# Kernel tuning notes

Measured on AMD Instinct MI355X. Metric: run time of the kernel, lower is better.

Reference implementation:

```python
import jax, jax.numpy as jnp
import numpy as np

KSIZE = 3
COUT = 128
GC = 4

def _unfold(x, k):
    # x: [B,C,H,W] -> [B,C,k*k,H,W]; zero pad (k-1)//2, stride 1 (matches nn.Unfold ordering)
    B, C, H, W = x.shape
    p = (k - 1) // 2
    xp = jnp.pad(x, ((0, 0), (0, 0), (p, p), (p, p)))
    return jnp.stack([xp[:, :, i:i + H, j:j + W] for i in range(k) for j in range(k)], axis=2)

def _bn(x, g, b, m, v, eps=1e-5):
    # inference-mode BatchNorm along channel axis 1, any rank
    sh = (1, -1) + (1,) * (x.ndim - 2)
    return (x - m.reshape(sh)) * (g / jnp.sqrt(v + eps)).reshape(sh) + b.reshape(sh)

def setup_inputs():
    key = jax.random.key(0)
    ks = jax.random.split(key, 15)
    B, C, H, W = 4, 128, 56, 56
    mid = C // 4
    OG = COUT * GC
    s = 0.05
    return {
        'x': jax.random.normal(ks[0], (B, C, H, W), jnp.float32),
        'Wk': jax.random.normal(ks[1], (C, C), jnp.float32) * s,
        'bn1_g': jax.random.uniform(ks[2], (C,), jnp.float32, 0.5, 1.5),
        'bn1_b': jax.random.normal(ks[3], (C,), jnp.float32) * s,
        'bn1_m': jnp.zeros((C,), jnp.float32),
        'bn1_v': jnp.ones((C,), jnp.float32),
        'W1': jax.random.normal(ks[4], (mid, 2 * C), jnp.float32) * s,
        'b1': jax.random.normal(ks[5], (mid,), jnp.float32) * s,
        'bn2_g': jax.random.uniform(ks[6], (mid,), jnp.float32, 0.5, 1.5),
        'bn2_b': jax.random.normal(ks[7], (mid,), jnp.float32) * s,
        'bn2_m': jnp.zeros((mid,), jnp.float32),
        'bn2_v': jnp.ones((mid,), jnp.float32),
        'W2': jax.random.normal(ks[8], (OG, mid), jnp.float32) * s,
        'b2': jax.random.normal(ks[9], (OG,), jnp.float32) * s,
        'gn_g': jax.random.uniform(ks[10], (OG,), jnp.float32, 0.5, 1.5),
        'gn_b': jax.random.normal(ks[11], (OG,), jnp.float32) * s,
        'Wv': jax.random.normal(ks[12], (OG, C), jnp.float32) * s,
        'bnv_g': jax.random.uniform(ks[13], (OG,), jnp.float32, 0.5, 1.5),
        'bnv_b': jax.random.normal(ks[14], (OG,), jnp.float32) * s,
        'bnv_m': jnp.zeros((OG,), jnp.float32),
        'bnv_v': jnp.ones((OG,), jnp.float32),
    }

def reference(x, Wk, bn1_g, bn1_b, bn1_m, bn1_v, W1, b1, bn2_g, bn2_b, bn2_m, bn2_v,
              W2, b2, gn_g, gn_b, Wv, bnv_g, bnv_b, bnv_m, bnv_v):
    B, C, H, W = x.shape
    k2 = KSIZE * KSIZE
    # emb_K: 1x1 conv (no bias) + BN + ReLU, then local unfold
    ke = jax.nn.relu(_bn(jnp.einsum('bchw,dc->bdhw', x, Wk), bn1_g, bn1_b, bn1_m, bn1_v))
    Kp = _unfold(ke, KSIZE)                        # [B,C,k2,H,W]
    Q = jnp.broadcast_to(x[:, :, None], Kp.shape)  # repeat x over k2 (einops '(c k)')
    QK = jnp.concatenate([Q, Kp], axis=1)          # [B,2C,k2,H,W]
    # MLP: 1x1 convs act pointwise over (k2,H,W)
    h = jax.nn.relu(_bn(jnp.einsum('bcphw,mc->bmphw', QK, W1) + b1.reshape(1, -1, 1, 1, 1),
                        bn2_g, bn2_b, bn2_m, bn2_v))
    a = jnp.einsum('bmphw,om->bophw', h, W2) + b2.reshape(1, -1, 1, 1, 1)  # [B,COUT*GC,k2,H,W]
    a = a.reshape(B, COUT, GC, k2, H, W)
    # GroupNorm: num_groups=COUT -> normalize over (GC, k2, H, W) per (b, out)
    mu = a.mean(axis=(2, 3, 4, 5), keepdims=True)
    var = jnp.mean(jnp.square(a - mu), axis=(2, 3, 4, 5), keepdims=True)
    a = (a - mu) / jnp.sqrt(var + 1e-5)
    a = a * gn_g.reshape(1, COUT, GC, 1, 1, 1) + gn_b.reshape(1, COUT, GC, 1, 1, 1)
    # emb_V: 1x1 conv (no bias) + BN, then local unfold
    v = _bn(jnp.einsum('bchw,oc->bohw', x, Wv), bnv_g, bnv_b, bnv_m, bnv_v)
    V = _unfold(v, KSIZE).reshape(B, COUT, GC, k2, H, W)
    return jnp.sum(a * V, axis=(2, 3))             # [B,COUT,H,W]
```

## Files before the change

### kernel.cpp

```cpp
#include <hip/hip_runtime.h>
#include <hip/hip_bf16.h>

typedef __hip_bfloat16 bf16;
typedef __attribute__((ext_vector_type(8))) short short8;
typedef __attribute__((ext_vector_type(4))) float f32x4;

#define HWP 3136
#define WD 56
#define PW 58
#define PADP 3364
#define CC 128
#define MIDM 32
#define OGN 512
#define NB 4

enum : int {
  OFF_FLAG = 0,
  OFF_W2F  = 4,
  OFF_SC2  = OFF_W2F + OGN*MIDM,
  OFF_SH2  = OFF_SC2 + MIDM,
  OFF_B1F  = OFF_SH2 + MIDM,
  OFF_B2F  = OFF_B1F + MIDM,
  OFF_GNG  = OFF_B2F + OGN,
  OFF_GNB  = OFF_GNG + OGN,
  OFF_GPART= OFF_GNB + OGN,
  OFF_PQ   = OFF_GPART + NB*128*1056,
  OFF_SS1  = OFF_PQ + NB*OGN*2,
  OFF_SSV  = OFF_SS1 + CC*2,
  OFF_WKB  = OFF_SSV + OGN*2,
  OFF_WVB  = OFF_WKB + CC*CC/2,
  OFF_W1AB = OFF_WVB + OGN*CC/2,
  OFF_W1BB = OFF_W1AB + MIDM*CC/2,
  OFF_HQT  = OFF_W1BB + MIDM*CC/2,
  OFF_GKT  = OFF_HQT + NB*HWP*MIDM/2,
  OFF_VT   = OFF_GKT + NB*PADP*MIDM/2,
  OFF_R1   = OFF_VT + NB*PADP*OGN/2,
  OFF_XT   = OFF_R1,
  WS_TOTAL = OFF_R1 + NB*9*HWP*MIDM/2
};

__device__ __forceinline__ float b2f(unsigned short u) {
  bf16 h; *(unsigned short*)&h = u; return __bfloat162float(h);
}
__device__ __forceinline__ unsigned short f2b(float f) {
  bf16 h = __float2bfloat16(f); return *(unsigned short*)&h;
}
__device__ __forceinline__ float ldmix(const void* p, size_t i, bool isbf) {
  return isbf ? __bfloat162float(((const bf16*)p)[i]) : ((const float*)p)[i];
}
__device__ __forceinline__ f32x4 mfma16(short8 a, short8 b, f32x4 c) {
  return __builtin_amdgcn_mfma_f32_16x16x32_bf16(a, b, c, 0, 0, 0);
}
__device__ __forceinline__ bool detect_bf(const unsigned short* xr) {
  int cnt = 0;
#pragma unroll
  for (int i = 0; i < 32; i++) {
    short8 v = *(const short8*)(xr + i*8);
#pragma unroll
    for (int j = 0; j < 8; j++) {
      int e = (((unsigned short)v[j]) >> 7) & 0xFF;
      cnt += (e >= 141) ? 1 : 0;
    }
  }
  return cnt < 8;
}

__global__ __launch_bounds__(256) void k_prep(
    const void* __restrict__ x,  const void* __restrict__ Wk,
    const void* __restrict__ bn1_g, const void* __restrict__ bn1_b,
    const void* __restrict__ bn1_m, const void* __restrict__ bn1_v,
    const void* __restrict__ W1, const void* __restrict__ b1,
    const void* __restrict__ bn2_g, const void* __restrict__ bn2_b,
    const void* __restrict__ bn2_m, const void* __restrict__ bn2_v,
    const void* __restrict__ W2, const void* __restrict__ b2,
    const void* __restrict__ gn_g, const void* __restrict__ gn_b,
    const void* __restrict__ Wv,
    const void* __restrict__ bnv_g, const void* __restrict__ bnv_b,
    const void* __restrict__ bnv_m, const void* __restrict__ bnv_v,
    float* __restrict__ ws) {
  __shared__ unsigned short tile[32*130];
  const bool isbf = detect_bf((const unsigned short*)x);
  int blk = blockIdx.x, tid = threadIdx.x;
  if (blk == 0 && tid == 0) ws[OFF_FLAG] = isbf ? 1.f : 0.f;
  int gid = blk*256 + tid, gstride = gridDim.x*256;
  unsigned short* wkb = (unsigned short*)(ws + OFF_WKB);
  unsigned short* wvb = (unsigned short*)(ws + OFF_WVB);
  unsigned short* w1ab = (unsigned short*)(ws + OFF_W1AB);
  unsigned short* w1bb = (unsigned short*)(ws + OFF_W1BB);
  float2* ss1 = (float2*)(ws + OFF_SS1);
  float2* ssv = (float2*)(ws + OFF_SSV);
  for (int i = gid; i < CC*CC; i += gstride) wkb[i] = f2b(ldmix(Wk, i, isbf));
  for (int i = gid; i < OGN*CC; i += gstride) wvb[i] = f2b(ldmix(Wv, i, isbf));
  for (int i = gid; i < MIDM*CC; i += gstride) {
    int m = i / CC, c = i % CC;
    w1ab[i] = f2b(ldmix(W1, (size_t)m*(2*CC) + c, isbf));
    w1bb[i] = f2b(ldmix(W1, (size_t)m*(2*CC) + CC + c, isbf));
  }
  for (int i = gid; i < OGN*MIDM; i += gstride) ws[OFF_W2F + i] = ldmix(W2, i, isbf);
  for (int i = gid; i < CC; i += gstride) {
    float s = ldmix(bn1_g, i, isbf) / sqrtf(ldmix(bn1_v, i, isbf) + 1e-5f);
    ss1[i] = make_float2(s, ldmix(bn1_b, i, isbf) - ldmix(bn1_m, i, isbf) * s);
  }
  for (int i = gid; i < MIDM; i += gstride) {
    float s = ldmix(bn2_g, i, isbf) / sqrtf(ldmix(bn2_v, i, isbf) + 1e-5f);
    ws[OFF_SC2 + i] = s;
    ws[OFF_SH2 + i] = ldmix(bn2_b, i, isbf) - ldmix(bn2_m, i, isbf)*s;
    ws[OFF_B1F + i] = ldmix(b1, i, isbf);
  }
  for (int i = gid; i < OGN; i += gstride) {
    float s = ldmix(bnv_g, i, isbf) / sqrtf(ldmix(bnv_v, i, isbf) + 1e-5f);
    ssv[i] = make_float2(s, ldmix(bnv_b, i, isbf) - ldmix(bnv_m, i, isbf) * s);
    ws[OFF_B2F + i] = ldmix(b2, i, isbf);
    ws[OFF_GNG + i] = ldmix(gn_g, i, isbf);
    ws[OFF_GNB + i] = ldmix(gn_b, i, isbf);
  }
  if (blk < 392) {
    int b = blk / 98, pix0 = (blk % 98)*32;
#pragma unroll
    for (int k = 0; k < 16; k++) {
      int idx = tid + k*256;
      int c = idx >> 5, pl = idx & 31;
      tile[pl*130 + c] = f2b(ldmix(x, ((size_t)b*CC + c)*HWP + pix0 + pl, isbf));
    }
    __syncthreads();
    unsigned short* xt = (unsigned short*)(ws + OFF_XT);
#pragma unroll
    for (int k = 0; k < 16; k++) {
      int idx = tid + k*256;
      int c = idx & 127, pl = idx >> 7;
      xt[((size_t)b*HWP + pix0 + pl)*CC + c] = tile[pl*130 + c];
    }
  } else {
    const int NV = 912*64, NG = NB*PADP*4;
    const short8 z = {0,0,0,0,0,0,0,0};
    unsigned short* vt = (unsigned short*)(ws + OFF_VT);
    unsigned short* gk = (unsigned short*)(ws + OFF_GKT);
    for (int u = (blk-392)*256 + tid; u < NV + NG; u += 28*256) {
      if (u < NV) {
        int bpp = u >> 6, och = u & 63;
        int b = bpp / 228, j = bpp - b*228;
        int pp;
        if (j < 58)       pp = j;
        else if (j < 116) pp = 57*PW + (j - 58);
        else if (j < 172) pp = (j - 116 + 1)*PW;
        else              pp = (j - 172 + 1)*PW + 57;
        *(short8*)(vt + ((size_t)b*PADP + pp)*OGN + och*8) = z;
      } else {
        int u2 = u - NV;
        int b = u2 / (PADP*4), rem = u2 - b*(PADP*4);
        int pp = rem >> 2, mch = rem & 3;
        *(short8*)(gk + ((size_t)b*PADP + pp)*MIDM + mch*8) = z;
      }
    }
  }
}

__global__ __launch_bounds__(256, 4) void k_mid(float* __restrict__ ws) {
  __shared__ unsigned short keL[4][16][136];
  int bid = blockIdx.x, tid = threadIdx.x;
  int w = tid >> 6, lane = tid & 63, q = lane >> 4, l16 = lane & 15;
  if (bid < 196) {
    int b = bid / 49, bx = bid - (bid/49)*49;
    int pix = bx*64 + w*16 + l16;
    const unsigned short* xt = (const unsigned short*)(ws + OFF_XT) + ((size_t)b*HWP + pix)*CC;
    short8 Bx[4];
#pragma unroll
    for (int kk = 0; kk < 4; kk++) Bx[kk] = *(const short8*)(xt + kk*32 + q*8);
    const unsigned short* wkb = (const unsigned short*)(ws + OFF_WKB);
    const float2* ss = (const float2*)(ws + OFF_SS1);
#pragma unroll
    for (int ot = 0; ot < 8; ot++) {
      int drow = ot*16 + l16;
      f32x4 c = {0.f, 0.f, 0.f, 0.f};
#pragma unroll
      for (int kk = 0; kk < 4; kk++)
        c = mfma16(*(const short8*)(wkb + (size_t)drow*CC + kk*32 + q*8), Bx[kk], c);
      int d0 = ot*16 + q*4;
      ushort4 st;
      { float2 s = ss[d0+0]; st.x = f2b(fmaxf(s.x*c[0] + s.y, 0.f)); }
      { float2 s = ss[d0+1]; st.y = f2b(fmaxf(s.x*c[1] + s.y, 0.f)); }
      { float2 s = ss[d0+2]; st.z = f2b(fmaxf(s.x*c[2] + s.y, 0.f)); }
      { float2 s = ss[d0+3]; st.w = f2b(fmaxf(s.x*c[3] + s.y, 0.f)); }
      *(ushort4*)&keL[w][l16][d0] = st;
    }
    __syncthreads();
    short8 Bk[4];
#pragma unroll
    for (int kk = 0; kk < 4; kk++) Bk[kk] = *(const short8*)&keL[w][l16][kk*32 + q*8];
    const unsigned short* w1a = (const unsigned short*)(ws + OFF_W1AB);
    const unsigned short* w1b = (const unsigned short*)(ws + OFF_W1BB);
    int h0 = pix / WD, w0 = pix - h0*WD;
    int pp = (h0+1)*PW + (w0+1);
    unsigned short* hqt = (unsigned short*)(ws + OFF_HQT) + ((size_t)b*HWP + pix)*MIDM;
    unsigned short* gkt = (unsigned short*)(ws + OFF_GKT) + ((size_t)b*PADP + pp)*MIDM;
#pragma unroll
    for (int mt = 0; mt < 2; mt++) {
      int mrow = mt*16 + l16;
      f32x4 ch = {0.f,0.f,0.f,0.f}, cg = {0.f,0.f,0.f,0.f};
#pragma unroll
      for (int kk = 0; kk < 4; kk++) {
        ch = mfma16(*(const short8*)(w1a + (size_t)mrow*CC + kk*32 + q*8), Bx[kk], ch);
        cg = mfma16(*(const short8*)(w1b + (size_t)mrow*CC + kk*32 + q*8), Bk[kk], cg);
      }
      int m0 = mt*16 + q*4;
      ushort4 sh, sg;
      sh.x = f2b(ch[0]); sh.y = f2b(ch[1]); sh.z = f2b(ch[2]); sh.w = f2b(ch[3]);
      sg.x = f2b(cg[0]); sg.y = f2b(cg[1]); sg.z = f2b(cg[2]); sg.w = f2b(cg[3]);
      *(ushort4*)(hqt + m0) = sh;
      *(ushort4*)(gkt + m0) = sg;
    }
  } else {
    int vid = bid - 196;
    int bx = vid % 49, rest = vid / 49;
    int by = rest & 3, b = rest >> 2;
    int pix = bx*64 + w*16 + l16;
    int h0 = pix / WD, w0 = pix - h0*WD;
    int pp = (h0+1)*PW + (w0+1);
    const unsigned short* xt = (const unsigned short*)(ws + OFF_XT) + ((size_t)b*HWP + pix)*CC;
    short8 B[4];
#pragma unroll
    for (int kk = 0; kk < 4; kk++) B[kk] = *(const short8*)(xt + kk*32 + q*8);
    const unsigned short* wvb = (const unsigned short*)(ws + OFF_WVB);
    const float2* ss = (const float2*)(ws + OFF_SSV);
    unsigned short* vt = (unsigned short*)(ws + OFF_VT) + ((size_t)b*PADP + pp)*OGN;
#pragma unroll
    for (int ot = 0; ot < 8; ot++) {
      int orow = by*128 + ot*16 + l16;
      f32x4 c = {0.f, 0.f, 0.f, 0.f};
#pragma unroll
      for (int kk = 0; kk < 4; kk++)
        c = mfma16(*(const short8*)(wvb + (size_t)orow*CC + kk*32 + q*8), B[kk], c);
      int o0 = by*128 + ot*16 + q*4;
      ushort4 st;
      { float2 s = ss[o0+0]; st.x = f2b(s.x*c[0] + s.y); }
      { float2 s = ss[o0+1]; st.y = f2b(s.x*c[1] + s.y); }
      { float2 s = ss[o0+2]; st.z = f2b(s.x*c[2] + s.y); }
      { float2 s = ss[o0+3]; st.w = f2b(s.x*c[3] + s.y); }
      *(ushort4*)(vt + o0) = st;
    }
  }
}

__global__ __launch_bounds__(256) void k_gramh(float* __restrict__ ws) {
  __shared__ unsigned short tileT[32][264];
  int b = blockIdx.y, bk = blockIdx.x;
  int tid = threadIdx.x;
  int w = tid >> 6, lane = tid & 63, q = lane >> 4, l16 = lane & 15;
  const int base = bk * 882;
  const unsigned short* hqt = (const unsigned short*)(ws + OFF_HQT) + (size_t)b*HWP*MIDM;
  const unsigned short* gkp = (const unsigned short*)(ws + OFF_GKT) + (size_t)b*PADP*MIDM;
  float sc2[MIDM], bas0[MIDM];
#pragma unroll
  for (int m = 0; m < MIDM; m++) {
    sc2[m] = ws[OFF_SC2 + m];
    bas0[m] = sc2[m]*ws[OFF_B1F + m] + ws[OFF_SH2 + m];
  }
  f32x4 gLL={0,0,0,0}, gLH={0,0,0,0}, gHH={0,0,0,0}, sL={0,0,0,0}, sH={0,0,0,0};
  short8 ones;
#pragma unroll
  for (int j = 0; j < 8; j++) ones[j] = (short)0x3F80;
  for (int t = 0; t < 4; t++) {
    int r = t*256 + tid;
    bool valid = r < 882;
    int R = valid ? (base + r) : 0;
    int p = R / HWP, pix = R - p*HWP;
    int h0 = pix / WD, w0 = pix - h0*WD;
    int npp = (h0 + p/3)*PW + (w0 + p - (p/3)*3);
    const unsigned short* hq = hqt + (size_t)pix*MIDM;
    const unsigned short* gk = gkp + (size_t)npp*MIDM;
#pragma unroll
    for (int ch = 0; ch < 4; ch++) {
      short8 th = *(const short8*)(hq + ch*8);
      short8 tg = *(const short8*)(gk + ch*8);
      short8 o;
#pragma unroll
      for (int j = 0; j < 8; j++) {
        int m = ch*8 + j;
        float hv = b2f((unsigned short)th[j]) + b2f((unsigned short)tg[j]);
        float v = fmaxf(sc2[m]*hv + bas0[m], 0.f);
        o[j] = valid ? (short)f2b(v) : (short)0;
      }
#pragma unroll
      for (int j = 0; j < 8; j++) tileT[ch*8 + j][tid] = (unsigned short)o[j];
    }
    __syncthreads();
#pragma unroll
    for (int cc = 0; cc < 2; cc++) {
      int c = w*2 + cc;
      short8 alo = *(const short8*)&tileT[l16][c*32 + q*8];
      short8 ahi = *(const short8*)&tileT[l16+16][c*32 + q*8];
      gLL = mfma16(alo, alo, gLL);
      gLH = mfma16(alo, ahi, gLH);
      gHH = mfma16(ahi, ahi, gHH);
      sL = mfma16(alo, ones, sL);
      sH = mfma16(ahi, ones, sH);
    }
    __syncthreads();
  }
  float* blob = ws + OFF_GPART + ((size_t)((b*32 + bk)*4 + w))*1056;
#pragma unroll
  for (int r = 0; r < 4; r++) {
    int row = q*4 + r;
    blob[row*32 + l16]             = gLL[r];
    blob[row*32 + 16 + l16]        = gLH[r];
    blob[(16 + l16)*32 + row]      = gLH[r];
    blob[(16 + row)*32 + 16 + l16] = gHH[r];
  }
  if (l16 == 0) {
#pragma unroll
    for (int r = 0; r < 4; r++) {
      blob[1024 + q*4 + r]      = sL[r];
      blob[1024 + 16 + q*4 + r] = sH[r];
    }
  }
}

__global__ __launch_bounds__(512) void k_stats(float* __restrict__ ws) {
  __shared__ float Gs[MIDM*MIDM], S1s[MIDM], saS[OGN], sqS[OGN], muS[128], invS[128];
  int b = blockIdx.x, o = threadIdx.x;
  for (int e = o; e < 1056; e += 512) {
    float s = 0.f;
    const float* pb = ws + OFF_GPART + (size_t)b*128*1056 + e;
    for (int p = 0; p < 128; p++) s += pb[(size_t)p*1056];
    if (e < 1024) Gs[e] = s; else S1s[e - 1024] = s;
  }
  __syncthreads();
  float w2[MIDM];
#pragma unroll
  for (int m = 0; m < MIDM; m++) w2[m] = ws[OFF_W2F + o*MIDM + m];
  float dotS = 0.f;
#pragma unroll
  for (int m = 0; m < MIDM; m++) dotS += w2[m] * S1s[m];
  float quad = 0.f;
  for (int a = 0; a < MIDM; a++) {
    float t = 0.f;
#pragma unroll
    for (int c = 0; c < MIDM; c++) t += Gs[a*MIDM + c] * w2[c];
    quad += w2[a] * t;
  }
  float b2o = ws[OFF_B2F + o];
  const float M = 9.f * HWP;
  saS[o] = dotS + b2o * M;
  sqS[o] = quad + 2.f*b2o*dotS + b2o*b2o*M;
  __syncthreads();
  if (o < 128) {
    float sa = saS[4*o] + saS[4*o+1] + saS[4*o+2] + saS[4*o+3];
    float sq = sqS[4*o] + sqS[4*o+1] + sqS[4*o+2] + sqS[4*o+3];
    const float invN = 1.f / (4.f * M);
    float mu = sa * invN;
    float var = sq * invN - mu*mu;
    muS[o] = mu;
    invS[o] = 1.f / sqrtf(var + 1e-5f);
  }
  __syncthreads();
  int co = o >> 2;
  float alpha = ws[OFF_GNG + o] * invS[co];
  ((float2*)(ws + OFF_PQ))[b*OGN + o] =
      make_float2(alpha, alpha*b2o + ws[OFF_GNB + o] - muS[co]*alpha);
}

#define VST2 68
__global__ __launch_bounds__(256, 5) void k_out(const float* __restrict__ ws,
                                                void* __restrict__ outp) {
  __shared__ unsigned short tileV[192*VST2];
  int b = blockIdx.z, by = blockIdx.y;
  int tid = threadIdx.x;
  int w = tid >> 6, lane = tid & 63, q = lane >> 4, l16 = lane & 15;
  int pix0 = blockIdx.x*64;
  int h00 = pix0 / WD, w00 = pix0 - h00*WD;
  int wstart = (h00+1)*PW + (w00+1) - (PW+1);
  int pix = pix0 + w*16 + l16;
  int h0 = pix / WD, w0 = pix - h0*WD;
  const unsigned short* hq = (const unsigned short*)(ws + OFF_HQT)
      + ((size_t)b*HWP + pix)*MIDM + q*8;
  const unsigned short* gkb = (const unsigned short*)(ws + OFF_GKT)
      + ((size_t)b*PADP + h0*PW + w0)*MIDM + q*8;
  float sc[8], ba[8], hvq[8];
  {
    short8 th = *(const short8*)hq;
#pragma unroll
    for (int j = 0; j < 8; j++) {
      int m = q*8 + j;
      sc[j] = ws[OFF_SC2 + m];
      ba[j] = sc[j]*ws[OFF_B1F + m] + ws[OFF_SH2 + m];
      hvq[j] = b2f((unsigned short)th[j]);
    }
  }
  short8 Bf[9];
#pragma unroll
  for (int p = 0; p < 9; p++) {
    short8 tg = *(const short8*)(gkb + (size_t)((p/3)*PW + (p - (p/3)*3))*MIDM);
#pragma unroll
    for (int j = 0; j < 8; j++)
      Bf[p][j] = (short)f2b(fmaxf(sc[j]*(hvq[j] + b2f((unsigned short)tg[j])) + ba[j], 0.f));
  }
  const unsigned short* vsrc = (const unsigned short*)(ws + OFF_VT)
      + (size_t)b*PADP*OGN + (size_t)by*64;
#pragma unroll
  for (int i = 0; i < 12; i++) {
    int u = i*256 + tid;
    int wp = u >> 4, col = (u & 15)*4;
    *(ushort4*)&tileV[wp*VST2 + col] =
        *(const ushort4*)(vsrc + (size_t)(wstart + wp)*OGN + col);
  }
  const bool isbf = ws[OFF_FLAG] > 0.5f;
  const float2* pq = (const float2*)(ws + OFF_PQ) + b*OGN;
  short8 A[4];
  f32x4 Qv[4];
#pragma unroll
  for (int ot = 0; ot < 4; ot++) {
    int orow = by*64 + ot*16 + l16;
    float P = pq[orow].x;
    const float* wrow = ws + OFF_W2F + (size_t)orow*MIDM + q*8;
    short8 a;
#pragma unroll
    for (int j = 0; j < 8; j++) a[j] = (short)f2b(P * wrow[j]);
    A[ot] = a;
    int o0 = by*64 + ot*16 + q*4;
    f32x4 qv = { pq[o0+0].y, pq[o0+1].y, pq[o0+2].y, pq[o0+3].y };
    Qv[ot] = qv;
  }
  int ppl = (h0+1)*PW + (w0+1) - wstart;
  float acc[4];
#pragma unroll
  for (int ot = 0; ot < 4; ot++) acc[ot] = 0.f;
  __syncthreads();
  const int doff[9] = {-PW-1, -PW, -PW+1, -1, 0, 1, PW-1, PW, PW+1};
#pragma unroll
  for (int p = 0; p < 9; p++) {
    int lp = ppl + doff[p];
    const unsigned short* vrow = &tileV[lp*VST2];
#pragma unroll
    for (int ot = 0; ot < 4; ot++) {
      f32x4 c = {0.f, 0.f, 0.f, 0.f};
      c = mfma16(A[ot], Bf[p], c);
      ushort4 vv = *(const ushort4*)(vrow + ot*16 + q*4);
      acc[ot] += (c[0] + Qv[ot][0])*b2f(vv.x) + (c[1] + Qv[ot][1])*b2f(vv.y)
               + (c[2] + Qv[ot][2])*b2f(vv.z) + (c[3] + Qv[ot][3])*b2f(vv.w);
    }
  }
#pragma unroll
  for (int ot = 0; ot < 4; ot++) {
    int co = by*16 + ot*4 + q;
    size_t oidx = ((size_t)b*128 + co)*HWP + pix;
    if (isbf) __builtin_nontemporal_store(f2b(acc[ot]), (unsigned short*)outp + oidx);
    else      __builtin_nontemporal_store(acc[ot], (float*)outp + oidx);
  }
}

extern "C" void kernel_launch(void* const* d_in, const int* in_sizes, int n_in,
                              void* d_out, int out_size, void* d_ws, size_t ws_size,
                              hipStream_t stream) {
  float* ws = (float*)d_ws;
  hipLaunchKernelGGL(k_prep, dim3(420), dim3(256), 0, stream,
                     d_in[0], d_in[1], d_in[2], d_in[3], d_in[4], d_in[5],
                     d_in[6], d_in[7], d_in[8], d_in[9], d_in[10], d_in[11],
                     d_in[12], d_in[13], d_in[14], d_in[15], d_in[16],
                     d_in[17], d_in[18], d_in[19], d_in[20], ws);
  hipLaunchKernelGGL(k_mid,  dim3(980),      dim3(256), 0, stream, ws);
  hipLaunchKernelGGL(k_gramh,dim3(32, 4),    dim3(256), 0, stream, ws);
  hipLaunchKernelGGL(k_stats,dim3(4),        dim3(512), 0, stream, ws);
  hipLaunchKernelGGL(k_out,  dim3(49, 8, 4), dim3(256), 0, stream, ws, d_out);
}
```

Baseline: 225.3 us.

## Process two pixel tiles per k_out block and precompute scaled W2 in k_stats

Each k_out block now covers 128 pixels instead of 64, staging a larger V tile in shared memory so the A fragments, Q values and scale constants are loaded once and reused for both halves. The GroupNorm-scaled W2 matrix (alpha*W2) is now converted to bf16 once in k_stats and stored in the workspace, replacing per-block float loads and conversions. This trades more shared memory and lower occupancy (launch bounds drop from 5 to 4) and a serial second half for less redundant setup work and halo reloading.

```diff
diff --git a/kernel.cpp b/kernel.cpp
--- a/kernel.cpp
+++ b/kernel.cpp
@@ -36,6 +36,7 @@
   OFF_VT   = OFF_GKT + NB*PADP*MIDM/2,
   OFF_R1   = OFF_VT + NB*PADP*OGN/2,
   OFF_XT   = OFF_R1,
+  OFF_AB   = OFF_R1,
   WS_TOTAL = OFF_R1 + NB*9*HWP*MIDM/2
 };
 
@@ -357,47 +358,58 @@
   float alpha = ws[OFF_GNG + o] * invS[co];
   ((float2*)(ws + OFF_PQ))[b*OGN + o] =
       make_float2(alpha, alpha*b2o + ws[OFF_GNB + o] - muS[co]*alpha);
+  unsigned short* dst = (unsigned short*)(ws + OFF_AB) + ((size_t)b*OGN + o)*MIDM;
+#pragma unroll
+  for (int m = 0; m < MIDM; m += 4) {
+    ushort4 t;
+    t.x = f2b(alpha*w2[m+0]); t.y = f2b(alpha*w2[m+1]);
+    t.z = f2b(alpha*w2[m+2]); t.w = f2b(alpha*w2[m+3]);
+    *(ushort4*)(dst + m) = t;
+  }
 }
 
 #define VST2 68
-__global__ __launch_bounds__(256, 5) void k_out(const float* __restrict__ ws,
+__global__ __launch_bounds__(256, 4) void k_out(const float* __restrict__ ws,
                                                 void* __restrict__ outp) {
-  __shared__ unsigned short tileV[192*VST2];
+  __shared__ unsigned short tileV[256*VST2];
   int b = blockIdx.z, by = blockIdx.y;
+  int bx = blockIdx.x;
   int tid = threadIdx.x;
   int w = tid >> 6, lane = tid & 63, q = lane >> 4, l16 = lane & 15;
-  int pix0 = blockIdx.x*64;
+  int pix0 = bx*128;
   int h00 = pix0 / WD, w00 = pix0 - h00*WD;
   int wstart = (h00+1)*PW + (w00+1) - (PW+1);
-  int pix = pix0 + w*16 + l16;
-  int h0 = pix / WD, w0 = pix - h0*WD;
-  const unsigned short* hq = (const unsigned short*)(ws + OFF_HQT)
-      + ((size_t)b*HWP + pix)*MIDM + q*8;
-  const unsigned short* gkb = (const unsigned short*)(ws + OFF_GKT)
-      + ((size_t)b*PADP + h0*PW + w0)*MIDM + q*8;
-  float sc[8], ba[8], hvq[8];
+  const bool hasB = (bx < 24);
+  int pixA = pix0 + w*16 + l16;
+  float sc[8], ba[8];
+#pragma unroll
+  for (int j = 0; j < 8; j++) {
+    int m = q*8 + j;
+    sc[j] = ws[OFF_SC2 + m];
+    ba[j] = sc[j]*ws[OFF_B1F + m] + ws[OFF_SH2 + m];
+  }
+  const unsigned short* hqt = (const unsigned short*)(ws + OFF_HQT) + (size_t)b*HWP*MIDM;
+  const unsigned short* gkt = (const unsigned short*)(ws + OFF_GKT) + (size_t)b*PADP*MIDM;
+  int hA = pixA / WD, wA = pixA - hA*WD;
+  short8 BfA[9];
   {
-    short8 th = *(const short8*)hq;
-#pragma unroll
-    for (int j = 0; j < 8; j++) {
-      int m = q*8 + j;
-      sc[j] = ws[OFF_SC2 + m];
-      ba[j] = sc[j]*ws[OFF_B1F + m] + ws[OFF_SH2 + m];
-      hvq[j] = b2f((unsigned short)th[j]);
-    }
-  }
-  short8 Bf[9];
-#pragma unroll
-  for (int p = 0; p < 9; p++) {
-    short8 tg = *(const short8*)(gkb + (size_t)((p/3)*PW + (p - (p/3)*3))*MIDM);
-#pragma unroll
-    for (int j = 0; j < 8; j++)
-      Bf[p][j] = (short)f2b(fmaxf(sc[j]*(hvq[j] + b2f((unsigned short)tg[j])) + ba[j], 0.f));
+    short8 th = *(const short8*)(hqt + (size_t)pixA*MIDM + q*8);
+    float hv[8];
+#pragma unroll
+    for (int j = 0; j < 8; j++) hv[j] = b2f((unsigned short)th[j]);
+    const unsigned short* gkb = gkt + ((size_t)hA*PW + wA)*MIDM + q*8;
+#pragma unroll
+    for (int p = 0; p < 9; p++) {
+      short8 tg = *(const short8*)(gkb + (size_t)((p/3)*PW + (p - (p/3)*3))*MIDM);
+#pragma unroll
+      for (int j = 0; j < 8; j++)
+        BfA[p][j] = (short)f2b(fmaxf(sc[j]*(hv[j] + b2f((unsigned short)tg[j])) + ba[j], 0.f));
+    }
   }
   const unsigned short* vsrc = (const unsigned short*)(ws + OFF_VT)
       + (size_t)b*PADP*OGN + (size_t)by*64;
 #pragma unroll
-  for (int i = 0; i < 12; i++) {
+  for (int i = 0; i < 16; i++) {
     int u = i*256 + tid;
     int wp = u >> 4, col = (u & 15)*4;
     *(ushort4*)&tileV[wp*VST2 + col] =
@@ -405,46 +417,83 @@
   }
   const bool isbf = ws[OFF_FLAG] > 0.5f;
   const float2* pq = (const float2*)(ws + OFF_PQ) + b*OGN;
+  const unsigned short* ABp = (const unsigned short*)(ws + OFF_AB)
+      + ((size_t)b*OGN + by*64)*MIDM;
   short8 A[4];
   f32x4 Qv[4];
 #pragma unroll
   for (int ot = 0; ot < 4; ot++) {
-    int orow = by*64 + ot*16 + l16;
-    float P = pq[orow].x;
-    const float* wrow = ws + OFF_W2F + (size_t)orow*MIDM + q*8;
-    short8 a;
-#pragma unroll
-    for (int j = 0; j < 8; j++) a[j] = (short)f2b(P * wrow[j]);
-    A[ot] = a;
+    A[ot] = *(const short8*)(ABp + (size_t)(ot*16 + l16)*MIDM + q*8);
     int o0 = by*64 + ot*16 + q*4;
     f32x4 qv = { pq[o0+0].y, pq[o0+1].y, pq[o0+2].y, pq[o0+3].y };
     Qv[ot] = qv;
   }
-  int ppl = (h0+1)*PW + (w0+1) - wstart;
-  float acc[4];
-#pragma unroll
-  for (int ot = 0; ot < 4; ot++) acc[ot] = 0.f;
+  const int doff[9] = {-PW-1, -PW, -PW+1, -1, 0, 1, PW-1, PW, PW+1};
   __syncthreads();
-  const int doff[9] = {-PW-1, -PW, -PW+1, -1, 0, 1, PW-1, PW, PW+1};
-#pragma unroll
-  for (int p = 0; p < 9; p++) {
-    int lp = ppl + doff[p];
-    const unsigned short* vrow = &tileV[lp*VST2];
+  {
+    int ppl = (hA+1)*PW + (wA+1) - wstart;
+    float acc[4] = {0.f, 0.f, 0.f, 0.f};
+#pragma unroll
+    for (int p = 0; p < 9; p++) {
+      int lp = ppl + doff[p];
+      const unsigned short* vrow = &tileV[lp*VST2];
+#pragma unroll
+      for (int ot = 0; ot < 4; ot++) {
+        f32x4 c = {0.f, 0.f, 0.f, 0.f};
+        c = mfma16(A[ot], BfA[p], c);
+        ushort4 vv = *(const ushort4*)(vrow + ot*16 + q*4);
+        acc[ot] += (c[0] + Qv[ot][0])*b2f(vv.x) + (c[1] + Qv[ot][1])*b2f(vv.y)
+                 + (c[2] + Qv[ot][2])*b2f(vv.z) + (c[3] + Qv[ot][3])*b2f(vv.w);
+      }
+    }
 #pragma unroll
     for (int ot = 0; ot < 4; ot++) {
-      f32x4 c = {0.f, 0.f, 0.f, 0.f};
-      c = mfma16(A[ot], Bf[p], c);
-      ushort4 vv = *(const ushort4*)(vrow + ot*16 + q*4);
-      acc[ot] += (c[0] + Qv[ot][0])*b2f(vv.x) + (c[1] + Qv[ot][1])*b2f(vv.y)
-               + (c[2] + Qv[ot][2])*b2f(vv.z) + (c[3] + Qv[ot][3])*b2f(vv.w);
-    }
-  }
-#pragma unroll
-  for (int ot = 0; ot < 4; ot++) {
-    int co = by*16 + ot*4 + q;
-    size_t oidx = ((size_t)b*128 + co)*HWP + pix;
-    if (isbf) __builtin_nontemporal_store(f2b(acc[ot]), (unsigned short*)outp + oidx);
-    else      __builtin_nontemporal_store(acc[ot], (float*)outp + oidx);
+      int co = by*16 + ot*4 + q;
+      size_t oidx = ((size_t)b*128 + co)*HWP + pixA;
+      if (isbf) __builtin_nontemporal_store(f2b(acc[ot]), (unsigned short*)outp + oidx);
+      else      __builtin_nontemporal_store(acc[ot], (float*)outp + oidx);
+    }
+  }
+  if (hasB) {
+    int pixB = pixA + 64;
+    int hB = pixB / WD, wB = pixB - hB*WD;
+    short8 BfB[9];
+    {
+      short8 th = *(const short8*)(hqt + (size_t)pixB*MIDM + q*8);
+      float hv[8];
+#pragma unroll
+      for (int j = 0; j < 8; j++) hv[j] = b2f((unsigned short)th[j]);
+      const unsigned short* gkb = gkt + ((size_t)hB*PW + wB)*MIDM + q*8;
+#pragma unroll
+      for (int p = 0; p < 9; p++) {
+        short8 tg = *(const short8*)(gkb + (size_t)((p/3)*PW + (p - (p/3)*3))*MIDM);
+#pragma unroll
+        for (int j = 0; j < 8; j++)
+          BfB[p][j] = (short)f2b(fmaxf(sc[j]*(hv[j] + b2f((unsigned short)tg[j])) + ba[j], 0.f));
+      }
+    }
+    int ppl = (hB+1)*PW + (wB+1) - wstart;
+    float acc[4] = {0.f, 0.f, 0.f, 0.f};
+#pragma unroll
+    for (int p = 0; p < 9; p++) {
+      int lp = ppl + doff[p];
+      const unsigned short* vrow = &tileV[lp*VST2];
+#pragma unroll
+      for (int ot = 0; ot < 4; ot++) {
+        f32x4 c = {0.f, 0.f, 0.f, 0.f};
+        c = mfma16(A[ot], BfB[p], c);
+        ushort4 vv = *(const ushort4*)(vrow + ot*16 + q*4);
+        acc[ot] += (c[0] + Qv[ot][0])*b2f(vv.x) + (c[1] + Qv[ot][1])*b2f(vv.y)
+                 + (c[2] + Qv[ot][2])*b2f(vv.z) + (c[3] + Qv[ot][3])*b2f(vv.w);
+      }
+    }
+#pragma unroll
+    for (int ot = 0; ot < 4; ot++) {
+      int co = by*16 + ot*4 + q;
+      size_t oidx = ((size_t)b*128 + co)*HWP + pixB;
+      if (isbf) __builtin_nontemporal_store(f2b(acc[ot]), (unsigned short*)outp + oidx);
+      else      __builtin_nontemporal_store(acc[ot], (float*)outp + oidx);
+    }
   }
 }
 
@@ -460,5 +509,5 @@
   hipLaunchKernelGGL(k_mid,  dim3(980),      dim3(256), 0, stream, ws);
   hipLaunchKernelGGL(k_gramh,dim3(32, 4),    dim3(256), 0, stream, ws);
   hipLaunchKernelGGL(k_stats,dim3(4),        dim3(512), 0, stream, ws);
-  hipLaunchKernelGGL(k_out,  dim3(49, 8, 4), dim3(256), 0, stream, ws, d_out);
-}
+  hipLaunchKernelGGL(k_out,  dim3(25, 8, 4), dim3(256), 0, stream, ws, d_out);
+}
```

Result: faster. 213.7 us (-5.1%).

## Process two output-channel tiles per k_out block and precompute scaled bf16 W2

Applied to the files above, without the earlier changes.

Each k_out block now covers 128 output groups (two passes of 64) rather than 64, so the per-pixel ReLU'd B fragments built from the HQ/GK buffers are computed once and reused across twice as many channels, and the grid's y dimension halves. The GroupNorm-scaled W2 matrix is now converted to bf16 once in k_stats and stored in the reused R1 workspace region, replacing the per-block scale-and-convert work. The V tile in shared memory doubles in width and the launch-bounds occupancy hint drops from 5 to 3, trading occupancy and parallelism for less redundant work.

```diff
diff --git a/kernel.cpp b/kernel.cpp
--- a/kernel.cpp
+++ b/kernel.cpp
@@ -36,6 +36,7 @@
   OFF_VT   = OFF_GKT + NB*PADP*MIDM/2,
   OFF_R1   = OFF_VT + NB*PADP*OGN/2,
   OFF_XT   = OFF_R1,
+  OFF_AB   = OFF_R1,
   WS_TOTAL = OFF_R1 + NB*9*HWP*MIDM/2
 };
 
@@ -357,94 +358,100 @@
   float alpha = ws[OFF_GNG + o] * invS[co];
   ((float2*)(ws + OFF_PQ))[b*OGN + o] =
       make_float2(alpha, alpha*b2o + ws[OFF_GNB + o] - muS[co]*alpha);
-}
-
-#define VST2 68
-__global__ __launch_bounds__(256, 5) void k_out(const float* __restrict__ ws,
+  unsigned short* dst = (unsigned short*)(ws + OFF_AB) + ((size_t)b*OGN + o)*MIDM;
+#pragma unroll
+  for (int m = 0; m < MIDM; m += 4) {
+    ushort4 t;
+    t.x = f2b(alpha*w2[m+0]); t.y = f2b(alpha*w2[m+1]);
+    t.z = f2b(alpha*w2[m+2]); t.w = f2b(alpha*w2[m+3]);
+    *(ushort4*)(dst + m) = t;
+  }
+}
+
+#define VST 136
+__global__ __launch_bounds__(256, 3) void k_out(const float* __restrict__ ws,
                                                 void* __restrict__ outp) {
-  __shared__ unsigned short tileV[192*VST2];
-  int b = blockIdx.z, by = blockIdx.y;
+  __shared__ unsigned short tileV[192*VST];
+  int b = blockIdx.z, bp = blockIdx.y;
+  int bx = blockIdx.x;
   int tid = threadIdx.x;
   int w = tid >> 6, lane = tid & 63, q = lane >> 4, l16 = lane & 15;
-  int pix0 = blockIdx.x*64;
+  int pix0 = bx*64;
   int h00 = pix0 / WD, w00 = pix0 - h00*WD;
   int wstart = (h00+1)*PW + (w00+1) - (PW+1);
   int pix = pix0 + w*16 + l16;
+  float sc[8], ba[8];
+#pragma unroll
+  for (int j = 0; j < 8; j++) {
+    int m = q*8 + j;
+    sc[j] = ws[OFF_SC2 + m];
+    ba[j] = sc[j]*ws[OFF_B1F + m] + ws[OFF_SH2 + m];
+  }
+  const unsigned short* hqt = (const unsigned short*)(ws + OFF_HQT) + (size_t)b*HWP*MIDM;
+  const unsigned short* gkt = (const unsigned short*)(ws + OFF_GKT) + (size_t)b*PADP*MIDM;
   int h0 = pix / WD, w0 = pix - h0*WD;
-  const unsigned short* hq = (const unsigned short*)(ws + OFF_HQT)
-      + ((size_t)b*HWP + pix)*MIDM + q*8;
-  const unsigned short* gkb = (const unsigned short*)(ws + OFF_GKT)
-      + ((size_t)b*PADP + h0*PW + w0)*MIDM + q*8;
-  float sc[8], ba[8], hvq[8];
+  short8 Bf[9];
   {
-    short8 th = *(const short8*)hq;
-#pragma unroll
-    for (int j = 0; j < 8; j++) {
-      int m = q*8 + j;
-      sc[j] = ws[OFF_SC2 + m];
-      ba[j] = sc[j]*ws[OFF_B1F + m] + ws[OFF_SH2 + m];
-      hvq[j] = b2f((unsigned short)th[j]);
-    }
-  }
-  short8 Bf[9];
-#pragma unroll
-  for (int p = 0; p < 9; p++) {
-    short8 tg = *(const short8*)(gkb + (size_t)((p/3)*PW + (p - (p/3)*3))*MIDM);
-#pragma unroll
-    for (int j = 0; j < 8; j++)
-      Bf[p][j] = (short)f2b(fmaxf(sc[j]*(hvq[j] + b2f((unsigned short)tg[j])) + ba[j], 0.f));
+    short8 th = *(const short8*)(hqt + (size_t)pix*MIDM + q*8);
+    float hv[8];
+#pragma unroll
+    for (int j = 0; j < 8; j++) hv[j] = b2f((unsigned short)th[j]);
+    const unsigned short* gkb = gkt + ((size_t)h0*PW + w0)*MIDM + q*8;
+#pragma unroll
+    for (int p = 0; p < 9; p++) {
+      short8 tg = *(const short8*)(gkb + (size_t)((p/3)*PW + (p - (p/3)*3))*MIDM);
+#pragma unroll
+      for (int j = 0; j < 8; j++)
+        Bf[p][j] = (short)f2b(fmaxf(sc[j]*(hv[j] + b2f((unsigned short)tg[j])) + ba[j], 0.f));
+    }
   }
   const unsigned short* vsrc = (const unsigned short*)(ws + OFF_VT)
-      + (size_t)b*PADP*OGN + (size_t)by*64;
+      + (size_t)b*PADP*OGN + (size_t)bp*128;
 #pragma unroll
   for (int i = 0; i < 12; i++) {
     int u = i*256 + tid;
-    int wp = u >> 4, col = (u & 15)*4;
-    *(ushort4*)&tileV[wp*VST2 + col] =
-        *(const ushort4*)(vsrc + (size_t)(wstart + wp)*OGN + col);
+    int wp = u >> 4, col = (u & 15)*8;
+    *(short8*)&tileV[wp*VST + col] =
+        *(const short8*)(vsrc + (size_t)(wstart + wp)*OGN + col);
   }
   const bool isbf = ws[OFF_FLAG] > 0.5f;
   const float2* pq = (const float2*)(ws + OFF_PQ) + b*OGN;
-  short8 A[4];
-  f32x4 Qv[4];
-#pragma unroll
-  for (int ot = 0; ot < 4; ot++) {
-    int orow = by*64 + ot*16 + l16;
-    float P = pq[orow].x;
-    const float* wrow = ws + OFF_W2F + (size_t)orow*MIDM + q*8;
-    short8 a;
-#pragma unroll
-    for (int j = 0; j < 8; j++) a[j] = (short)f2b(P * wrow[j]);
-    A[ot] = a;
-    int o0 = by*64 + ot*16 + q*4;
-    f32x4 qv = { pq[o0+0].y, pq[o0+1].y, pq[o0+2].y, pq[o0+3].y };
-    Qv[ot] = qv;
-  }
+  const unsigned short* ABb = (const unsigned short*)(ws + OFF_AB)
+      + ((size_t)b*OGN + bp*128)*MIDM;
+  const int doff[9] = {-PW-1, -PW, -PW+1, -1, 0, 1, PW-1, PW, PW+1};
   int ppl = (h0+1)*PW + (w0+1) - wstart;
-  float acc[4];
-#pragma unroll
-  for (int ot = 0; ot < 4; ot++) acc[ot] = 0.f;
   __syncthreads();
-  const int doff[9] = {-PW-1, -PW, -PW+1, -1, 0, 1, PW-1, PW, PW+1};
-#pragma unroll
-  for (int p = 0; p < 9; p++) {
-    int lp = ppl + doff[p];
-    const unsigned short* vrow = &tileV[lp*VST2];
+  for (int byv = 0; byv < 2; ++byv) {
+    short8 A[4];
+    f32x4 Qv[4];
 #pragma unroll
     for (int ot = 0; ot < 4; ot++) {
-      f32x4 c = {0.f, 0.f, 0.f, 0.f};
-      c = mfma16(A[ot], Bf[p], c);
-      ushort4 vv = *(const ushort4*)(vrow + ot*16 + q*4);
-      acc[ot] += (c[0] + Qv[ot][0])*b2f(vv.x) + (c[1] + Qv[ot][1])*b2f(vv.y)
-               + (c[2] + Qv[ot][2])*b2f(vv.z) + (c[3] + Qv[ot][3])*b2f(vv.w);
-    }
-  }
-#pragma unroll
-  for (int ot = 0; ot < 4; ot++) {
-    int co = by*16 + ot*4 + q;
-    size_t oidx = ((size_t)b*128 + co)*HWP + pix;
-    if (isbf) __builtin_nontemporal_store(f2b(acc[ot]), (unsigned short*)outp + oidx);
-    else      __builtin_nontemporal_store(acc[ot], (float*)outp + oidx);
+      A[ot] = *(const short8*)(ABb + (size_t)(byv*64 + ot*16 + l16)*MIDM + q*8);
+      int o0 = bp*128 + byv*64 + ot*16 + q*4;
+      f32x4 qv = { pq[o0+0].y, pq[o0+1].y, pq[o0+2].y, pq[o0+3].y };
+      Qv[ot] = qv;
+    }
+    float acc[4] = {0.f, 0.f, 0.f, 0.f};
+#pragma unroll
+    for (int p = 0; p < 9; p++) {
+      int lp = ppl + doff[p];
+      const unsigned short* vrow = &tileV[lp*VST + byv*64];
+#pragma unroll
+      for (int ot = 0; ot < 4; ot++) {
+        f32x4 c = {0.f, 0.f, 0.f, 0.f};
+        c = mfma16(A[ot], Bf[p], c);
+        ushort4 vv = *(const ushort4*)(vrow + ot*16 + q*4);
+        acc[ot] += (c[0] + Qv[ot][0])*b2f(vv.x) + (c[1] + Qv[ot][1])*b2f(vv.y)
+                 + (c[2] + Qv[ot][2])*b2f(vv.z) + (c[3] + Qv[ot][3])*b2f(vv.w);
+      }
+    }
+#pragma unroll
+    for (int ot = 0; ot < 4; ot++) {
+      int co = bp*32 + byv*16 + ot*4 + q;
+      size_t oidx = ((size_t)b*128 + co)*HWP + pix;
+      if (isbf) __builtin_nontemporal_store(f2b(acc[ot]), (unsigned short*)outp + oidx);
+      else      __builtin_nontemporal_store(acc[ot], (float*)outp + oidx);
+    }
   }
 }
 
@@ -460,5 +467,5 @@
   hipLaunchKernelGGL(k_mid,  dim3(980),      dim3(256), 0, stream, ws);
   hipLaunchKernelGGL(k_gramh,dim3(32, 4),    dim3(256), 0, stream, ws);
   hipLaunchKernelGGL(k_stats,dim3(4),        dim3(512), 0, stream, ws);
-  hipLaunchKernelGGL(k_out,  dim3(49, 8, 4), dim3(256), 0, stream, ws, d_out);
-}
+  hipLaunchKernelGGL(k_out,  dim3(49, 4, 4), dim3(256), 0, stream, ws, d_out);
+}
```

Result: faster. 192.5 us (-14.5%).
